# Kernel tuning notes

Hardware: AMD Instinct MI355X
Metric: run time of the kernel (lower is better)

## Reference

```python
import jax, jax.numpy as jnp
import numpy as np

EPS = 1e-4      # scn.BatchNormLeakyReLU default eps
LEAK = 0.333    # scn default leakiness

B, P, H, Wd = 4, 1, 640, 1024
N_PER = 100_000
CIN = COUT = 128
K = 9  # 1x3x3 stencil


def _build_rulebook(rng):
    # Sample unique active voxels per event, then hash-join neighbors (vectorized).
    coords = []
    for b in range(B):
        flat = rng.choice(P * H * Wd, size=N_PER, replace=False)
        p = flat // (H * Wd)
        r = flat % (H * Wd)
        coords.append(np.stack([np.full(N_PER, b), p, r // Wd, r % Wd], axis=1))
    coords = np.concatenate(coords).astype(np.int64)  # [N,4] = (b,p,y,x)
    N = coords.shape[0]
    # flat key with +1 padding in y,x so offsets never alias across borders
    keys = ((coords[:, 0] * P + coords[:, 1]) * (H + 2) + (coords[:, 2] + 1)) * (Wd + 2) + (coords[:, 3] + 1)
    order = np.argsort(keys)
    sk = keys[order]
    offsets = [(dy, dx) for dy in (-1, 0, 1) for dx in (-1, 0, 1)]
    neigh = np.full((N, K), N, dtype=np.int32)  # sentinel N -> zero row
    for k, (dy, dx) in enumerate(offsets):
        qk = keys + dy * (Wd + 2) + dx
        pos = np.searchsorted(sk, qk)
        posc = np.clip(pos, 0, N - 1)
        found = sk[posc] == qk
        neigh[:, k] = np.where(found, order[posc].astype(np.int32), np.int32(N))
    return neigh


def setup_inputs() -> dict:
    rng = np.random.default_rng(0)
    neigh_idx = jnp.asarray(_build_rulebook(rng))  # [N,9] int32
    key = jax.random.key(0)
    k1, k2, k3 = jax.random.split(key, 3)
    N = B * N_PER
    feats = jax.random.normal(k1, (N, CIN), dtype=jnp.float32)
    W = jax.random.normal(k2, (K, CIN, COUT), dtype=jnp.float32) * 0.05
    bias = jax.random.normal(k3, (COUT,), dtype=jnp.float32) * 0.01
    gamma = jnp.ones((COUT,), dtype=jnp.float32)
    beta = jnp.zeros((COUT,), dtype=jnp.float32)
    return {"feats": feats, "W": W, "bias": bias, "gamma": gamma, "beta": beta,
            "neigh_idx": neigh_idx}


def reference(feats, W, bias, gamma, beta, neigh_idx):
    # Submanifold sparse conv: gather active neighbors per kernel tap, GEMM, accumulate.
    N = feats.shape[0]
    fp = jnp.concatenate([feats, jnp.zeros((1, feats.shape[1]), feats.dtype)], axis=0)  # zero row for missing neighbors
    out = jnp.broadcast_to(bias, (N, W.shape[2])).astype(feats.dtype)
    for k in range(K):  # fixed small loop over kernel taps
        out = out + fp[neigh_idx[:, k]] @ W[k]  # [N,Cin] @ [Cin,Cout]
    # BatchNorm (training stats over active sites) + LeakyReLU, fused
    mean = out.mean(axis=0)
    var = out.var(axis=0)
    y = (out - mean) * jax.lax.rsqrt(var + EPS) * gamma + beta
    return jnp.where(y > 0, y, LEAK * y)
```

## Files before the change

### kernel.cpp

```cpp
#include <hip/hip_runtime.h>
#include <hip/hip_bf16.h>
#include <stdint.h>

#define N_PTS 400000
#define K_TAPS 9
#define CIN 128
#define COUT 128
#define EPS_BN 1e-4f
#define LEAK 0.333f

typedef __bf16 bf16x8 __attribute__((ext_vector_type(8)));
typedef float floatx16 __attribute__((ext_vector_type(16)));

#define PACKW_BYTES (K_TAPS * 8 * 4 * 64 * 8 * 2)
#define SUMS_OFF PACKW_BYTES
#define SUMSQ_OFF (SUMS_OFF + 512)
#define AB_OFF (SUMSQ_OFF + 512)
#define FEATSB_OFF (AB_OFF + 1024)
#define PREBN_OFF (FEATSB_OFF + (size_t)N_PTS * CIN * 2)
#define WS_NEED_A (PREBN_OFF + (size_t)N_PTS * COUT * 2)

__device__ inline unsigned int pack_bf16_rn(float lo, float hi) {
    unsigned int a = __float_as_uint(lo) + 0x8000u;
    unsigned int b = __float_as_uint(hi) + 0x8000u;
    return (a >> 16) | (b & 0xffff0000u);
}

__device__ inline void gload_lds16(const void* g, void* l) {
    __builtin_amdgcn_global_load_lds(
        (const __attribute__((address_space(1))) unsigned int*)g,
        (__attribute__((address_space(3))) unsigned int*)l, 16, 0, 0);
}

__global__ __launch_bounds__(256) void convert_feats_kernel(
    const float* __restrict__ f, __hip_bfloat16* __restrict__ o) {
    size_t i = ((size_t)blockIdx.x * 256 + threadIdx.x) * 16;
    const float4* f4 = (const float4*)(f + i);
    float4 a = f4[0], b = f4[1], c = f4[2], d = f4[3];
    uint4 v0, v1;
    v0.x = pack_bf16_rn(a.x, a.y);
    v0.y = pack_bf16_rn(a.z, a.w);
    v0.z = pack_bf16_rn(b.x, b.y);
    v0.w = pack_bf16_rn(b.z, b.w);
    v1.x = pack_bf16_rn(c.x, c.y);
    v1.y = pack_bf16_rn(c.z, c.w);
    v1.z = pack_bf16_rn(d.x, d.y);
    v1.w = pack_bf16_rn(d.z, d.w);
    *(uint4*)(o + i) = v0;
    *(uint4*)(o + i + 8) = v1;
}

__global__ void pack_w_kernel(const float* __restrict__ W,
                              __hip_bfloat16* __restrict__ pw,
                              float* __restrict__ gsum) {
    if (blockIdx.x == 288) {
        ((float4*)gsum)[threadIdx.x] = make_float4(0.f, 0.f, 0.f, 0.f);
        return;
    }
    int frag = blockIdx.x;
    int lane = threadIdx.x;
    int t = frag & 3;
    int c = (frag >> 2) & 7;
    int k = frag >> 5;
    int n = lane & 31;
    int kk0 = (lane >> 5) * 8;
    const float* src = W + (size_t)k * CIN * COUT + (size_t)(c * 16 + kk0) * COUT + (t * 32 + n);
    __hip_bfloat16* dst = pw + (size_t)frag * 512 + lane * 8;
#pragma unroll
    for (int j = 0; j < 8; ++j) dst[j] = (__hip_bfloat16)src[(size_t)j * COUT];
}

__device__ inline void stage_tap(char* smem, const char* pwb, int k, int buf,
                                 int wave, int lane) {
    const char* g = pwb + (size_t)k * 32768;
    char* l = smem + buf * 32768;
#pragma unroll
    for (int i = 0; i < 4; ++i) {
        int chunk = i * 8 + wave;
        gload_lds16(g + (size_t)chunk * 1024 + (size_t)lane * 16, l + (size_t)chunk * 1024);
    }
}

template <bool GATHER_BF16, bool OUT_BF16>
__global__ __launch_bounds__(512, 4) void spconv_gemm_kernel(
    const void* __restrict__ feats_any,
    const __hip_bfloat16* __restrict__ packw,
    const int* __restrict__ neigh,
    void* __restrict__ out_any,
    float* __restrict__ gsum, float* __restrict__ gsumsq) {
    __shared__ __align__(16) char smem[65536];

    const int tid = threadIdx.x;
    const int wave = tid >> 6;
    const int lane = tid & 63;
    const int hj = lane >> 5;
    const int m = lane & 31;
    const int row = blockIdx.x * 256 + wave * 32 + m;
    const bool rvalid = (row < N_PTS);
    const size_t nbase = (size_t)row * K_TAPS;

    floatx16 acc[4];
#pragma unroll
    for (int t = 0; t < 4; ++t)
#pragma unroll
        for (int r = 0; r < 16; ++r) acc[t][r] = 0.0f;

    const char* pwb = (const char*)packw;
    const __hip_bfloat16* fb = (const __hip_bfloat16*)feats_any;

    int nb[K_TAPS];
    uint4 avf[2][4];

    stage_tap(smem, pwb, 0, 0, wave, lane);
    if (GATHER_BF16) {
        nb[0] = rvalid ? neigh[nbase + 0] : N_PTS;
        nb[1] = rvalid ? neigh[nbase + 1] : N_PTS;
        {
            int s0 = (nb[0] < N_PTS) ? nb[0] : 0;
            const uint4* ar = (const uint4*)(fb + (size_t)s0 * CIN);
#pragma unroll
            for (int c = 0; c < 4; ++c) avf[0][c] = ar[c * 2 + hj];
        }
    } else {
#pragma unroll
        for (int k = 0; k < K_TAPS; ++k)
            nb[k] = rvalid ? neigh[nbase + k] : N_PTS;
    }
    __syncthreads();

#pragma unroll
    for (int k = 0; k < K_TAPS; ++k) {
        const int cur = k & 1;
        const int nbc = nb[k];
        const bool vcur = (nbc < N_PTS);
        const int safec = vcur ? nbc : 0;

        uint4 avs[4];
        uint4 a8[8];

        if (GATHER_BF16) {
            const uint4* ar = (const uint4*)(fb + (size_t)safec * CIN);
#pragma unroll
            for (int c = 0; c < 4; ++c) avs[c] = ar[(c + 4) * 2 + hj];

            if (k + 1 < K_TAPS) stage_tap(smem, pwb, k + 1, cur ^ 1, wave, lane);

            if (k + 1 < K_TAPS) {
                int nbn = nb[k + 1];
                int sn = (nbn < N_PTS) ? nbn : 0;
                const uint4* arn = (const uint4*)(fb + (size_t)sn * CIN);
#pragma unroll
                for (int c = 0; c < 4; ++c) avf[(k + 1) & 1][c] = arn[c * 2 + hj];
            }
            if (k + 2 < K_TAPS)
                nb[k + 2] = rvalid ? neigh[nbase + k + 2] : N_PTS;

            if (!vcur) {
#pragma unroll
                for (int c = 0; c < 4; ++c) {
                    avf[cur][c].x = 0u; avf[cur][c].y = 0u; avf[cur][c].z = 0u; avf[cur][c].w = 0u;
                    avs[c].x = 0u; avs[c].y = 0u; avs[c].z = 0u; avs[c].w = 0u;
                }
            }
        } else {
            const float4* ar = (const float4*)((const float*)feats_any + (size_t)safec * CIN);
#pragma unroll
            for (int c = 0; c < 8; ++c) {
                float4 f0 = ar[c * 4 + hj * 2];
                float4 f1 = ar[c * 4 + hj * 2 + 1];
                a8[c].x = pack_bf16_rn(f0.x, f0.y);
                a8[c].y = pack_bf16_rn(f0.z, f0.w);
                a8[c].z = pack_bf16_rn(f1.x, f1.y);
                a8[c].w = pack_bf16_rn(f1.z, f1.w);
            }
            if (k + 1 < K_TAPS) stage_tap(smem, pwb, k + 1, cur ^ 1, wave, lane);
            if (!vcur) {
#pragma unroll
                for (int c = 0; c < 8; ++c) { a8[c].x = 0u; a8[c].y = 0u; a8[c].z = 0u; a8[c].w = 0u; }
            }
        }

        const char* bbase = smem + cur * 32768;
        __builtin_amdgcn_s_setprio(1);
#pragma unroll
        for (int c = 0; c < 8; ++c) {
            uint4 araw;
            if (GATHER_BF16)
                araw = (c < 4) ? avf[cur][c] : avs[c - 4];
            else
                araw = a8[c];
            bf16x8 afrag = __builtin_bit_cast(bf16x8, araw);
#pragma unroll
            for (int t = 0; t < 4; ++t) {
                bf16x8 bfrag = __builtin_bit_cast(
                    bf16x8, *(const uint4*)(bbase + (c * 4 + t) * 1024 + lane * 16));
                acc[t] = __builtin_amdgcn_mfma_f32_32x32x16_bf16(afrag, bfrag, acc[t], 0, 0, 0);
            }
        }
        __builtin_amdgcn_s_setprio(0);

        __syncthreads();
    }

#pragma unroll
    for (int t = 0; t < 4; ++t) {
#pragma unroll
        for (int r = 0; r < 16; ++r) {
            int row_local = (r & 3) + 8 * (r >> 2) + 4 * hj;
            size_t grow = (size_t)blockIdx.x * 256 + wave * 32 + row_local;
            if (grow < N_PTS) {
                if (OUT_BF16)
                    ((__hip_bfloat16*)out_any)[grow * COUT + (t * 32 + m)] =
                        (__hip_bfloat16)acc[t][r];
                else
                    ((float*)out_any)[grow * COUT + (t * 32 + m)] = acc[t][r];
            }
        }
    }

    float s[4], q[4];
#pragma unroll
    for (int t = 0; t < 4; ++t) {
        s[t] = 0.0f; q[t] = 0.0f;
#pragma unroll
        for (int r = 0; r < 16; ++r) {
            float v = acc[t][r];
            s[t] += v;
            q[t] += v * v;
        }
        s[t] += __shfl_xor(s[t], 32, 64);
        q[t] += __shfl_xor(q[t], 32, 64);
    }

    float* lsum = (float*)smem;
    float* lsq = (float*)(smem + 4096);
    if (hj == 0) {
#pragma unroll
        for (int t = 0; t < 4; ++t) {
            lsum[wave * 128 + t * 32 + m] = s[t];
            lsq[wave * 128 + t * 32 + m] = q[t];
        }
    }
    __syncthreads();
    if (tid < 128) {
        float ts = 0.0f, tq = 0.0f;
#pragma unroll
        for (int w = 0; w < 8; ++w) {
            ts += lsum[w * 128 + tid];
            tq += lsq[w * 128 + tid];
        }
        atomicAdd(&gsum[tid], ts);
        atomicAdd(&gsumsq[tid], tq);
    }
}

__global__ __launch_bounds__(256) void bn_lrelu_bf16_kernel(
    const __hip_bfloat16* __restrict__ pre, float* __restrict__ out,
    const float* __restrict__ gsum, const float* __restrict__ gsumsq,
    const float* __restrict__ gamma, const float* __restrict__ beta) {
    __shared__ float ab[256];
    const int tid = threadIdx.x;
    if (tid < 128) {
        const float inv_n = 1.0f / (float)N_PTS;
        float mean = gsum[tid] * inv_n;
        float var = gsumsq[tid] * inv_n - mean * mean;
        float a = gamma[tid] * rsqrtf(var + EPS_BN);
        ab[tid] = a;
        ab[128 + tid] = beta[tid] - mean * a;
    }
    __syncthreads();

    size_t i = ((size_t)blockIdx.x * 256 + tid) * 16;
    int c0 = (int)(i & (COUT - 1));
    uint4 v0 = *(const uint4*)(pre + i);
    uint4 v1 = *(const uint4*)(pre + i + 8);
    unsigned int u[8] = {v0.x, v0.y, v0.z, v0.w, v1.x, v1.y, v1.z, v1.w};
    float o[16];
#pragma unroll
    for (int w = 0; w < 8; ++w) {
        float x0 = __uint_as_float((u[w] & 0xffffu) << 16);
        float x1 = __uint_as_float((u[w] >> 16) << 16);
        int c = c0 + 2 * w;
        float y0 = fmaf(ab[c], x0, ab[128 + c]);
        float y1 = fmaf(ab[c + 1], x1, ab[128 + c + 1]);
        o[2 * w] = (y0 > 0.0f) ? y0 : LEAK * y0;
        o[2 * w + 1] = (y1 > 0.0f) ? y1 : LEAK * y1;
    }
#pragma unroll
    for (int w = 0; w < 4; ++w)
        *(float4*)(out + i + 4 * w) =
            make_float4(o[4 * w], o[4 * w + 1], o[4 * w + 2], o[4 * w + 3]);
}

__global__ __launch_bounds__(256) void bn_lrelu_f32_kernel(
    float* __restrict__ out,
    const float* __restrict__ gsum, const float* __restrict__ gsumsq,
    const float* __restrict__ gamma, const float* __restrict__ beta) {
    __shared__ float ab[256];
    const int tid = threadIdx.x;
    if (tid < 128) {
        const float inv_n = 1.0f / (float)N_PTS;
        float mean = gsum[tid] * inv_n;
        float var = gsumsq[tid] * inv_n - mean * mean;
        float a = gamma[tid] * rsqrtf(var + EPS_BN);
        ab[tid] = a;
        ab[128 + tid] = beta[tid] - mean * a;
    }
    __syncthreads();

    size_t i = ((size_t)blockIdx.x * 256 + tid) * 8;
    int c0 = (int)(i & (COUT - 1));
#pragma unroll
    for (int h = 0; h < 2; ++h) {
        float4 v = *(const float4*)(out + i + 4 * h);
        int c = c0 + 4 * h;
        v.x = fmaf(ab[c], v.x, ab[128 + c]);
        v.y = fmaf(ab[c + 1], v.y, ab[128 + c + 1]);
        v.z = fmaf(ab[c + 2], v.z, ab[128 + c + 2]);
        v.w = fmaf(ab[c + 3], v.w, ab[128 + c + 3]);
        v.x = (v.x > 0.0f) ? v.x : LEAK * v.x;
        v.y = (v.y > 0.0f) ? v.y : LEAK * v.y;
        v.z = (v.z > 0.0f) ? v.z : LEAK * v.z;
        v.w = (v.w > 0.0f) ? v.w : LEAK * v.w;
        *(float4*)(out + i + 4 * h) = v;
    }
}

extern "C" void kernel_launch(void* const* d_in, const int* in_sizes, int n_in,
                              void* d_out, int out_size, void* d_ws, size_t ws_size,
                              hipStream_t stream) {
    const float* feats = (const float*)d_in[0];
    const float* W = (const float*)d_in[1];
    const float* gamma = (const float*)d_in[3];
    const float* beta = (const float*)d_in[4];
    const int* neigh = (const int*)d_in[5];
    float* out = (float*)d_out;

    char* ws = (char*)d_ws;
    __hip_bfloat16* packw = (__hip_bfloat16*)ws;
    float* gsum = (float*)(ws + SUMS_OFF);
    float* gsumsq = (float*)(ws + SUMSQ_OFF);

    const int gemm_grid = (N_PTS + 255) / 256;

    hipLaunchKernelGGL(pack_w_kernel, dim3(289), dim3(64), 0, stream, W, packw, gsum);

    if (ws_size >= WS_NEED_A) {
        __hip_bfloat16* featsb = (__hip_bfloat16*)(ws + FEATSB_OFF);
        __hip_bfloat16* prebn = (__hip_bfloat16*)(ws + PREBN_OFF);
        hipLaunchKernelGGL(convert_feats_kernel, dim3(12500), dim3(256), 0, stream, feats, featsb);
        hipLaunchKernelGGL((spconv_gemm_kernel<true, true>), dim3(gemm_grid), dim3(512), 0,
                           stream, (const void*)featsb, packw, neigh, (void*)prebn, gsum, gsumsq);
        hipLaunchKernelGGL(bn_lrelu_bf16_kernel, dim3(12500), dim3(256), 0, stream,
                           prebn, out, gsum, gsumsq, gamma, beta);
    } else {
        hipLaunchKernelGGL((spconv_gemm_kernel<false, false>), dim3(gemm_grid), dim3(512), 0,
                           stream, (const void*)feats, packw, neigh, (void*)out, gsum, gsumsq);
        hipLaunchKernelGGL(bn_lrelu_f32_kernel, dim3(50000), dim3(256), 0, stream,
                           out, gsum, gsumsq, gamma, beta);
    }
}
```

Before: 557.3 us.

## Pad zero feature row and software-pipeline neighbor gathers with explicit waitcnt

Adds a zero row after the bf16 feature copy so missing neighbors index it directly instead of being masked with per-tap selects and zeroing. Restructures the bf16 GEMM loop to prefetch the next tap's full A row interleaved with the MFMAs, using sched_barrier and a manual vmcnt wait plus s_barrier in place of __syncthreads. Also makes the final BN output stores nontemporal. The hand-written waitcnt depends on the exact count of outstanding loads and could be fragile if the compiler reorders or adds loads.

```diff
diff --git a/kernel.cpp b/kernel.cpp
--- a/kernel.cpp
+++ b/kernel.cpp
@@ -11,13 +11,14 @@
 
 typedef __bf16 bf16x8 __attribute__((ext_vector_type(8)));
 typedef float floatx16 __attribute__((ext_vector_type(16)));
+typedef float f32x4 __attribute__((ext_vector_type(4)));
 
 #define PACKW_BYTES (K_TAPS * 8 * 4 * 64 * 8 * 2)
 #define SUMS_OFF PACKW_BYTES
 #define SUMSQ_OFF (SUMS_OFF + 512)
 #define AB_OFF (SUMSQ_OFF + 512)
 #define FEATSB_OFF (AB_OFF + 1024)
-#define PREBN_OFF (FEATSB_OFF + (size_t)N_PTS * CIN * 2)
+#define PREBN_OFF (FEATSB_OFF + (size_t)(N_PTS + 1) * CIN * 2)
 #define WS_NEED_A (PREBN_OFF + (size_t)N_PTS * COUT * 2)
 
 __device__ inline unsigned int pack_bf16_rn(float lo, float hi) {
@@ -34,6 +35,13 @@
 
 __global__ __launch_bounds__(256) void convert_feats_kernel(
     const float* __restrict__ f, __hip_bfloat16* __restrict__ o) {
+    if (blockIdx.x == 12500) {
+        if (threadIdx.x < 16) {
+            uint4 z = {0u, 0u, 0u, 0u};
+            *(uint4*)(o + (size_t)N_PTS * CIN + threadIdx.x * 8) = z;
+        }
+        return;
+    }
     size_t i = ((size_t)blockIdx.x * 256 + threadIdx.x) * 16;
     const float4* f4 = (const float4*)(f + i);
     float4 a = f4[0], b = f4[1], c = f4[2], d = f4[3];
@@ -106,64 +114,73 @@
         for (int r = 0; r < 16; ++r) acc[t][r] = 0.0f;
 
     const char* pwb = (const char*)packw;
-    const __hip_bfloat16* fb = (const __hip_bfloat16*)feats_any;
-
-    int nb[K_TAPS];
-    uint4 avf[2][4];
-
-    stage_tap(smem, pwb, 0, 0, wave, lane);
-    if (GATHER_BF16) {
-        nb[0] = rvalid ? neigh[nbase + 0] : N_PTS;
-        nb[1] = rvalid ? neigh[nbase + 1] : N_PTS;
+
+    if constexpr (GATHER_BF16) {
+        const __hip_bfloat16* fb = (const __hip_bfloat16*)feats_any;
+        uint4 av[8];
+        int nbA, nbB;
+
+        nbA = rvalid ? neigh[nbase + 0] : N_PTS;
+        nbB = rvalid ? neigh[nbase + 1] : N_PTS;
+        stage_tap(smem, pwb, 0, 0, wave, lane);
+        __builtin_amdgcn_sched_barrier(0);
         {
-            int s0 = (nb[0] < N_PTS) ? nb[0] : 0;
-            const uint4* ar = (const uint4*)(fb + (size_t)s0 * CIN);
-#pragma unroll
-            for (int c = 0; c < 4; ++c) avf[0][c] = ar[c * 2 + hj];
+            const uint4* ar = (const uint4*)(fb + (size_t)nbA * CIN);
+#pragma unroll
+            for (int c = 0; c < 8; ++c) av[c] = ar[c * 2 + hj];
+        }
+        __builtin_amdgcn_sched_barrier(0);
+        asm volatile("s_waitcnt vmcnt(8)" ::: "memory");
+        __builtin_amdgcn_s_barrier();
+
+#pragma unroll
+        for (int k = 0; k < K_TAPS; ++k) {
+            const int cur = k & 1;
+            if (k + 2 < K_TAPS) {
+                int v = rvalid ? neigh[nbase + k + 2] : N_PTS;
+                if (cur == 0) nbA = v; else nbB = v;
+            }
+            if (k + 1 < K_TAPS) stage_tap(smem, pwb, k + 1, cur ^ 1, wave, lane);
+            __builtin_amdgcn_sched_barrier(0);
+
+            const char* bbase = smem + (size_t)cur * 32768;
+            const int nbn = (cur == 0) ? nbB : nbA;
+            const uint4* arn = (const uint4*)(fb + (size_t)nbn * CIN);
+
+            __builtin_amdgcn_s_setprio(1);
+#pragma unroll
+            for (int c = 0; c < 8; ++c) {
+                bf16x8 afrag = __builtin_bit_cast(bf16x8, av[c]);
+#pragma unroll
+                for (int t = 0; t < 4; ++t) {
+                    bf16x8 bfrag = __builtin_bit_cast(
+                        bf16x8, *(const uint4*)(bbase + (c * 4 + t) * 1024 + lane * 16));
+                    acc[t] = __builtin_amdgcn_mfma_f32_32x32x16_bf16(afrag, bfrag, acc[t], 0, 0, 0);
+                }
+                if (k + 1 < K_TAPS) av[c] = arn[c * 2 + hj];
+            }
+            __builtin_amdgcn_s_setprio(0);
+            __builtin_amdgcn_sched_barrier(0);
+
+            if (k + 1 < K_TAPS) {
+                asm volatile("s_waitcnt vmcnt(8)" ::: "memory");
+                __builtin_amdgcn_s_barrier();
+            }
         }
     } else {
+        int nb[K_TAPS];
 #pragma unroll
         for (int k = 0; k < K_TAPS; ++k)
             nb[k] = rvalid ? neigh[nbase + k] : N_PTS;
-    }
-    __syncthreads();
-
-#pragma unroll
-    for (int k = 0; k < K_TAPS; ++k) {
-        const int cur = k & 1;
-        const int nbc = nb[k];
-        const bool vcur = (nbc < N_PTS);
-        const int safec = vcur ? nbc : 0;
-
-        uint4 avs[4];
-        uint4 a8[8];
-
-        if (GATHER_BF16) {
-            const uint4* ar = (const uint4*)(fb + (size_t)safec * CIN);
-#pragma unroll
-            for (int c = 0; c < 4; ++c) avs[c] = ar[(c + 4) * 2 + hj];
-
-            if (k + 1 < K_TAPS) stage_tap(smem, pwb, k + 1, cur ^ 1, wave, lane);
-
-            if (k + 1 < K_TAPS) {
-                int nbn = nb[k + 1];
-                int sn = (nbn < N_PTS) ? nbn : 0;
-                const uint4* arn = (const uint4*)(fb + (size_t)sn * CIN);
-#pragma unroll
-                for (int c = 0; c < 4; ++c) avf[(k + 1) & 1][c] = arn[c * 2 + hj];
-            }
-            if (k + 2 < K_TAPS)
-                nb[k + 2] = rvalid ? neigh[nbase + k + 2] : N_PTS;
-
-            if (!vcur) {
-#pragma unroll
-                for (int c = 0; c < 4; ++c) {
-                    avf[cur][c].x = 0u; avf[cur][c].y = 0u; avf[cur][c].z = 0u; avf[cur][c].w = 0u;
-                    avs[c].x = 0u; avs[c].y = 0u; avs[c].z = 0u; avs[c].w = 0u;
-                }
-            }
-        } else {
-            const float4* ar = (const float4*)((const float*)feats_any + (size_t)safec * CIN);
+        stage_tap(smem, pwb, 0, 0, wave, lane);
+        __syncthreads();
+#pragma unroll
+        for (int k = 0; k < K_TAPS; ++k) {
+            const int cur = k & 1;
+            const bool valid = (nb[k] < N_PTS);
+            const int safe = valid ? nb[k] : 0;
+            uint4 a8[8];
+            const float4* ar = (const float4*)((const float*)feats_any + (size_t)safe * CIN);
 #pragma unroll
             for (int c = 0; c < 8; ++c) {
                 float4 f0 = ar[c * 4 + hj * 2];
@@ -174,33 +191,26 @@
                 a8[c].w = pack_bf16_rn(f1.z, f1.w);
             }
             if (k + 1 < K_TAPS) stage_tap(smem, pwb, k + 1, cur ^ 1, wave, lane);
-            if (!vcur) {
+            if (!valid) {
 #pragma unroll
                 for (int c = 0; c < 8; ++c) { a8[c].x = 0u; a8[c].y = 0u; a8[c].z = 0u; a8[c].w = 0u; }
             }
-        }
-
-        const char* bbase = smem + cur * 32768;
-        __builtin_amdgcn_s_setprio(1);
-#pragma unroll
-        for (int c = 0; c < 8; ++c) {
-            uint4 araw;
-            if (GATHER_BF16)
-                araw = (c < 4) ? avf[cur][c] : avs[c - 4];
-            else
-                araw = a8[c];
-            bf16x8 afrag = __builtin_bit_cast(bf16x8, araw);
-#pragma unroll
-            for (int t = 0; t < 4; ++t) {
-                bf16x8 bfrag = __builtin_bit_cast(
-                    bf16x8, *(const uint4*)(bbase + (c * 4 + t) * 1024 + lane * 16));
-                acc[t] = __builtin_amdgcn_mfma_f32_32x32x16_bf16(afrag, bfrag, acc[t], 0, 0, 0);
-            }
-        }
-        __builtin_amdgcn_s_setprio(0);
-
-        __syncthreads();
-    }
+            const char* bbase = smem + (size_t)cur * 32768;
+#pragma unroll
+            for (int c = 0; c < 8; ++c) {
+                bf16x8 afrag = __builtin_bit_cast(bf16x8, a8[c]);
+#pragma unroll
+                for (int t = 0; t < 4; ++t) {
+                    bf16x8 bfrag = __builtin_bit_cast(
+                        bf16x8, *(const uint4*)(bbase + (c * 4 + t) * 1024 + lane * 16));
+                    acc[t] = __builtin_amdgcn_mfma_f32_32x32x16_bf16(afrag, bfrag, acc[t], 0, 0, 0);
+                }
+            }
+            __syncthreads();
+        }
+    }
+
+    __syncthreads();
 
 #pragma unroll
     for (int t = 0; t < 4; ++t) {
@@ -287,9 +297,10 @@
         o[2 * w + 1] = (y1 > 0.0f) ? y1 : LEAK * y1;
     }
 #pragma unroll
-    for (int w = 0; w < 4; ++w)
-        *(float4*)(out + i + 4 * w) =
-            make_float4(o[4 * w], o[4 * w + 1], o[4 * w + 2], o[4 * w + 3]);
+    for (int w = 0; w < 4; ++w) {
+        f32x4 vv = {o[4 * w], o[4 * w + 1], o[4 * w + 2], o[4 * w + 3]};
+        __builtin_nontemporal_store(vv, (f32x4*)(out + i + 4 * w));
+    }
 }
 
 __global__ __launch_bounds__(256) void bn_lrelu_f32_kernel(
@@ -348,7 +359,7 @@
     if (ws_size >= WS_NEED_A) {
         __hip_bfloat16* featsb = (__hip_bfloat16*)(ws + FEATSB_OFF);
         __hip_bfloat16* prebn = (__hip_bfloat16*)(ws + PREBN_OFF);
-        hipLaunchKernelGGL(convert_feats_kernel, dim3(12500), dim3(256), 0, stream, feats, featsb);
+        hipLaunchKernelGGL(convert_feats_kernel, dim3(12501), dim3(256), 0, stream, feats, featsb);
         hipLaunchKernelGGL((spconv_gemm_kernel<true, true>), dim3(gemm_grid), dim3(512), 0,
                            stream, (const void*)featsb, packw, neigh, (void*)prebn, gsum, gsumsq);
         hipLaunchKernelGGL(bn_lrelu_bf16_kernel, dim3(12500), dim3(256), 0, stream,
```

Result: slower. 613.8 us (+10.1%).
